# Optimization experiments

Measured on AMD Instinct MI355X. Metric: run time of the kernel, lower is better.

The kernel has to match this reference:

```python
import jax, jax.numpy as jnp
import numpy as np
import math

HIDDEN = 256
N_HEADS = 4
MAX_NB = 64  # max neighbors per sample (segment length cap)
B = 4096
N_TOTAL = 131072


def setup_inputs() -> dict:
    key = jax.random.key(0)
    ks = jax.random.split(key, 12)
    enc_hidden = jax.random.normal(ks[0], (B, HIDDEN), dtype=jnp.float32)
    social_ht = jax.random.normal(ks[1], (N_TOTAL, HIDDEN), dtype=jnp.float32)
    # contiguous ragged segments: start in [0, N_TOTAL-MAX_NB], len in [1, MAX_NB]
    starts = jnp.sort(jax.random.randint(ks[2], (B,), 0, N_TOTAL - MAX_NB, dtype=jnp.int32))
    lens = jax.random.randint(ks[3], (B,), 1, MAX_NB + 1, dtype=jnp.int32)
    ends = starts + lens
    s = 1.0 / math.sqrt(HIDDEN)
    def lin(k):
        kw, kb = jax.random.split(k)
        W = jax.random.uniform(kw, (HIDDEN, HIDDEN), jnp.float32, -s, s)
        b = jax.random.uniform(kb, (HIDDEN,), jnp.float32, -s, s)
        return W, b
    Wq, bq = lin(ks[4])
    Wk, bk = lin(ks[5])
    Wv, bv = lin(ks[6])
    Wf, bf = lin(ks[7])
    return {
        "enc_hidden": enc_hidden, "social_ht": social_ht,
        "Wq": Wq, "bq": bq, "Wk": Wk, "bk": bk, "Wv": Wv, "bv": bv,
        "Wf": Wf, "bf": bf,
        "neighbors_idx_start": starts, "neighbors_idx_end": ends,
    }


def reference(enc_hidden, social_ht, Wq, bq, Wk, bk, Wv, bv, Wf, bf,
              neighbors_idx_start, neighbors_idx_end):
    b, h = enc_hidden.shape
    dh = h // N_HEADS
    # query: Linear+ReLU then scale by sqrt(feat_dim) (as in source)
    q = jax.nn.relu(enc_hidden @ Wq.T + bq) / jnp.sqrt(jnp.float32(h))  # [B,H]
    # gather padded contiguous neighbor segments
    idx = neighbors_idx_start[:, None] + jnp.arange(MAX_NB, dtype=neighbors_idx_start.dtype)  # [B,M]
    valid = idx < neighbors_idx_end[:, None]  # [B,M]
    ht = social_ht[jnp.clip(idx, 0, social_ht.shape[0] - 1)]  # [B,M,H]
    k = jax.nn.relu(ht @ Wk.T + bk)  # [B,M,H]
    v = jax.nn.relu(ht @ Wv.T + bv)  # [B,M,H]
    qh = q.reshape(b, N_HEADS, dh)            # [B,h,d]
    kh = k.reshape(b, MAX_NB, N_HEADS, dh)    # [B,M,h,d]
    vh = v.reshape(b, MAX_NB, N_HEADS, dh)
    scores = jnp.einsum('bhd,bmhd->bhm', qh, kh)
    scores = jnp.where(valid[:, None, :], scores, jnp.float32(-1e30))
    attn = jax.nn.softmax(scores, axis=-1)    # [B,h,M]
    out = jnp.einsum('bhm,bmhd->bhd', attn, vh).reshape(b, h)
    return out @ Wf.T + bf
```

## Files before the change

kernel.cpp:

```cpp
#include <hip/hip_runtime.h>
#include <hip/hip_bf16.h>

typedef __attribute__((ext_vector_type(8))) short bf16x8;
typedef __attribute__((ext_vector_type(4))) float f32x4;
typedef __attribute__((ext_vector_type(4))) unsigned short us4;

__device__ __forceinline__ unsigned short f2bf(float f) {
    unsigned int u = __builtin_bit_cast(unsigned int, f);
    unsigned int r = (u + 0x7FFFu + ((u >> 16) & 1u)) >> 16;
    return (unsigned short)r;
}
__device__ __forceinline__ float bf2f(unsigned short h) {
    unsigned int u = ((unsigned int)h) << 16;
    return __builtin_bit_cast(float, u);
}

__device__ __forceinline__ void gload_lds16(const void* g, void* l) {
    __builtin_amdgcn_global_load_lds(
        (const __attribute__((address_space(1))) unsigned int*)g,
        (__attribute__((address_space(3))) unsigned int*)l, 16, 0, 0);
}

__global__ __launch_bounds__(512, 2) void kv_gemm_rb(
    const float* __restrict__ A,
    const float* __restrict__ Wk, const float* __restrict__ bk,
    const float* __restrict__ Wv, const float* __restrict__ bv,
    unsigned short* __restrict__ KV)
{
    __shared__ unsigned short Abuf[2][32 * 256];

    const int tid = threadIdx.x;
    const int wave = tid >> 6, lane = tid & 63;
    const size_t mb = (size_t)blockIdx.x * 512;

    bf16x8 bfrag[4][8];
    float biasv[4];
    #pragma unroll
    for (int ni = 0; ni < 4; ++ni) {
        int col = wave * 64 + ni * 16 + (lane & 15);
        const float* Wr = (col < 256) ? (Wk + (size_t)col * 256)
                                      : (Wv + (size_t)(col - 256) * 256);
        biasv[ni] = (col < 256) ? bk[col] : bv[col - 256];
        #pragma unroll
        for (int ks = 0; ks < 8; ++ks) {
            int k0 = ks * 32 + ((lane >> 4) << 3);
            float4 x = *(const float4*)(Wr + k0);
            float4 y = *(const float4*)(Wr + k0 + 4);
            bf16x8 f;
            f[0] = (short)f2bf(x.x); f[1] = (short)f2bf(x.y);
            f[2] = (short)f2bf(x.z); f[3] = (short)f2bf(x.w);
            f[4] = (short)f2bf(y.x); f[5] = (short)f2bf(y.y);
            f[6] = (short)f2bf(y.z); f[7] = (short)f2bf(y.w);
            bfrag[ni][ks] = f;
        }
    }

    {
        const int row = tid >> 4, seg = tid & 15;
        const float* src = A + (mb + row) * 256 + seg * 16;
        float4 a0 = *(const float4*)(src + 0);
        float4 a1 = *(const float4*)(src + 4);
        float4 a2 = *(const float4*)(src + 8);
        float4 a3 = *(const float4*)(src + 12);
        us4 h0, h1, h2, h3;
        h0.x=f2bf(a0.x); h0.y=f2bf(a0.y); h0.z=f2bf(a0.z); h0.w=f2bf(a0.w);
        h1.x=f2bf(a1.x); h1.y=f2bf(a1.y); h1.z=f2bf(a1.z); h1.w=f2bf(a1.w);
        h2.x=f2bf(a2.x); h2.y=f2bf(a2.y); h2.z=f2bf(a2.z); h2.w=f2bf(a2.w);
        h3.x=f2bf(a3.x); h3.y=f2bf(a3.y); h3.z=f2bf(a3.z); h3.w=f2bf(a3.w);
        char* dst = (char*)Abuf[0];
        int byte0 = row * 512 + seg * 32;
        int sw = (row & 7) << 4;
        *(us4*)(dst + ((byte0 +  0) ^ sw)) = h0;
        *(us4*)(dst + ((byte0 + 16) ^ sw)) = h1;
        *(us4*)(dst + ((byte0 + 0 + 16) ^ sw)) = h1;
        char* d2 = dst;
        *(us4*)(d2 + ((byte0 + 0) ^ sw)) = h0;
        *(us4*)(d2 + ((byte0 + 16) ^ sw)) = h1;
        *(us4*)(d2 + ((byte0 +  0) ^ sw)) = h0;
        *(us4*)(d2 + ((byte0 +  8) ^ sw)) = h1;
        *(us4*)(d2 + ((byte0 + 16) ^ sw)) = h2;
        *(us4*)(d2 + ((byte0 + 24) ^ sw)) = h3;
    }
    __syncthreads();

    for (int t = 0; t < 16; ++t) {
        const int cur = t & 1;
        const bool pf = (t + 1) < 16;
        float4 a0, a1, a2, a3;
        if (pf) {
            const int row = tid >> 4, seg = tid & 15;
            const float* src = A + (mb + (t + 1) * 32 + row) * 256 + seg * 16;
            a0 = *(const float4*)(src + 0);
            a1 = *(const float4*)(src + 4);
            a2 = *(const float4*)(src + 8);
            a3 = *(const float4*)(src + 12);
        }

        f32x4 acc[2][4] = {};
        const char* Ab = (const char*)Abuf[cur];
        #pragma unroll
        for (int ks = 0; ks < 8; ++ks) {
            bf16x8 af[2];
            #pragma unroll
            for (int mi = 0; mi < 2; ++mi) {
                int row = mi * 16 + (lane & 15);
                int byte = row * 512 + ks * 64 + ((lane >> 4) << 4);
                af[mi] = *(const bf16x8*)(Ab + (byte ^ ((row & 7) << 4)));
            }
            #pragma unroll
            for (int ni = 0; ni < 4; ++ni)
                #pragma unroll
                for (int mi = 0; mi < 2; ++mi)
                    acc[mi][ni] = __builtin_amdgcn_mfma_f32_16x16x32_bf16(
                        af[mi], bfrag[ni][ks], acc[mi][ni], 0, 0, 0);
        }

        #pragma unroll
        for (int ni = 0; ni < 4; ++ni) {
            int col = wave * 64 + ni * 16 + (lane & 15);
            #pragma unroll
            for (int mi = 0; mi < 2; ++mi) {
                size_t rbase = mb + (size_t)t * 32 + mi * 16 + ((lane >> 4) << 2);
                #pragma unroll
                for (int r = 0; r < 4; ++r) {
                    float v = fmaxf(acc[mi][ni][r] + biasv[ni], 0.f);
                    KV[(rbase + r) * 512 + col] = f2bf(v);
                }
            }
        }

        if (pf) {
            const int row = tid >> 4, seg = tid & 15;
            us4 h0, h1, h2, h3;
            h0.x=f2bf(a0.x); h0.y=f2bf(a0.y); h0.z=f2bf(a0.z); h0.w=f2bf(a0.w);
            h1.x=f2bf(a1.x); h1.y=f2bf(a1.y); h1.z=f2bf(a1.z); h1.w=f2bf(a1.w);
            h2.x=f2bf(a2.x); h2.y=f2bf(a2.y); h2.z=f2bf(a2.z); h2.w=f2bf(a2.w);
            h3.x=f2bf(a3.x); h3.y=f2bf(a3.y); h3.z=f2bf(a3.z); h3.w=f2bf(a3.w);
            char* dst = (char*)Abuf[cur ^ 1];
            int byte0 = row * 512 + seg * 32;
            int sw = (row & 7) << 4;
            *(us4*)(dst + ((byte0 +  0) ^ sw)) = h0;
            *(us4*)(dst + ((byte0 +  8) ^ sw)) = h1;
            *(us4*)(dst + ((byte0 + 16) ^ sw)) = h2;
            *(us4*)(dst + ((byte0 + 24) ^ sw)) = h3;
        }
        __syncthreads();
    }
}

template<int OUT_BF16, int RELU>
__global__ __launch_bounds__(256) void gemm_proj(
    const float* __restrict__ A, int M,
    const float* __restrict__ W0, const float* __restrict__ b0,
    const float* __restrict__ W1, const float* __restrict__ b1,
    void* __restrict__ outp, int ncol, float scale)
{
    __shared__ unsigned short As[128 * 64];
    __shared__ unsigned short Bs[64 * 64];
    char* AsB = (char*)As;
    char* BsB = (char*)Bs;

    const int tid = threadIdx.x;
    const int wave = tid >> 6, lane = tid & 63;
    const int m0 = blockIdx.x * 128;
    const int jbase = blockIdx.y * 64;

    f32x4 acc[2][4] = {};

    for (int kk = 0; kk < 256; kk += 64) {
        #pragma unroll
        for (int i = 0; i < 8; ++i) {
            int fidx = tid + i * 256;
            int row = fidx >> 4;
            int col4 = (fidx & 15) << 2;
            const float4 v = *(const float4*)(A + (size_t)(m0 + row) * 256 + kk + col4);
            us4 h; h.x = f2bf(v.x); h.y = f2bf(v.y); h.z = f2bf(v.z); h.w = f2bf(v.w);
            int byte = row * 128 + col4 * 2;
            *(us4*)(AsB + (byte ^ ((row & 7) << 4))) = h;
        }
        #pragma unroll
        for (int i = 0; i < 4; ++i) {
            int fidx = tid + i * 256;
            int row = fidx >> 4;
            int col4 = (fidx & 15) << 2;
            int j = jbase + row;
            const float* W = (j < 256) ? (W0 + (size_t)j * 256) : (W1 + (size_t)(j - 256) * 256);
            const float4 v = *(const float4*)(W + kk + col4);
            us4 h; h.x = f2bf(v.x); h.y = f2bf(v.y); h.z = f2bf(v.z); h.w = f2bf(v.w);
            int byte = row * 128 + col4 * 2;
            *(us4*)(BsB + (byte ^ ((row & 7) << 4))) = h;
        }
        __syncthreads();
        #pragma unroll
        for (int k2 = 0; k2 < 2; ++k2) {
            const int kbyte = k2 * 64 + ((lane >> 4) << 4);
            bf16x8 af[2];
            #pragma unroll
            for (int mi = 0; mi < 2; ++mi) {
                int row = wave * 32 + mi * 16 + (lane & 15);
                int byte = row * 128 + kbyte;
                af[mi] = *(const bf16x8*)(AsB + (byte ^ ((row & 7) << 4)));
            }
            #pragma unroll
            for (int ni = 0; ni < 4; ++ni) {
                int row = ni * 16 + (lane & 15);
                int byte = row * 128 + kbyte;
                bf16x8 bfr = *(const bf16x8*)(BsB + (byte ^ ((row & 7) << 4)));
                #pragma unroll
                for (int mi = 0; mi < 2; ++mi)
                    acc[mi][ni] = __builtin_amdgcn_mfma_f32_16x16x32_bf16(af[mi], bfr, acc[mi][ni], 0, 0, 0);
            }
        }
        __syncthreads();
    }

    #pragma unroll
    for (int ni = 0; ni < 4; ++ni) {
        int col = ni * 16 + (lane & 15);
        int j = jbase + col;
        float bias = (j < 256) ? b0[j] : b1[j - 256];
        #pragma unroll
        for (int mi = 0; mi < 2; ++mi) {
            int rbase = m0 + wave * 32 + mi * 16 + ((lane >> 4) << 2);
            #pragma unroll
            for (int r = 0; r < 4; ++r) {
                float v = acc[mi][ni][r] + bias;
                if (RELU) v = fmaxf(v, 0.f);
                v *= scale;
                size_t off = (size_t)(rbase + r) * ncol + j;
                if (OUT_BF16) ((unsigned short*)outp)[off] = f2bf(v);
                else ((float*)outp)[off] = v;
            }
        }
    }
}

__global__ __launch_bounds__(256) void attn_kernel(
    const float* __restrict__ Q, const unsigned short* __restrict__ KV,
    const int* __restrict__ starts, const int* __restrict__ ends,
    float* __restrict__ out)
{
    extern __shared__ char lds[];
    char* kv = lds;
    float* awl = (float*)(lds + 65536);
    float* qs  = (float*)(lds + 65536 + 1024);

    const int bid = blockIdx.x;
    const int b = ((bid & 7) << 9) + (bid >> 3);
    const int t = threadIdx.x;
    const int h = t >> 6, ln = t & 63;
    const int start = starts[b];
    const int len = ends[b] - start;

    #pragma unroll
    for (int i = 0; i < 16; ++i) {
        int r = h * 16 + i;
        const char* src = (const char*)KV + (size_t)(start + r) * 1024;
        int sb = (ln * 16) ^ ((r & 7) << 4);
        gload_lds16(src + sb, kv + r * 1024 + ln * 16);
    }
    qs[t] = Q[(size_t)b * 256 + t];
    __syncthreads();

    float2 qreg[32];
    #pragma unroll
    for (int j = 0; j < 32; ++j)
        qreg[j] = *(const float2*)(qs + h * 64 + 2 * j);

    float sx = 0.f, sy = 0.f;
    {
        const char* krow = kv + ln * 1024;
        const int sw = (ln & 7) << 4;
        #pragma unroll
        for (int j8 = 0; j8 < 8; ++j8) {
            bf16x8 kf = *(const bf16x8*)(krow + (((h * 128) + j8 * 16) ^ sw));
            #pragma unroll
            for (int p = 0; p < 4; ++p) {
                float2 q2 = qreg[j8 * 4 + p];
                sx = fmaf(q2.x, bf2f((unsigned short)kf[2 * p]), sx);
                sy = fmaf(q2.y, bf2f((unsigned short)kf[2 * p + 1]), sy);
            }
        }
    }
    float s = (ln < len) ? (sx + sy) : -3.0e38f;
    float mx = s;
    #pragma unroll
    for (int off = 32; off; off >>= 1) mx = fmaxf(mx, __shfl_xor(mx, off));
    float e = (ln < len) ? __expf(s - mx) : 0.f;
    float sum = e;
    #pragma unroll
    for (int off = 32; off; off >>= 1) sum += __shfl_xor(sum, off);
    awl[h * 64 + ln] = e / sum;
    __syncthreads();

    const int half = ln >> 5, dl = ln & 31;
    float a0 = 0.f, a1 = 0.f;
    {
        const char* vbase = kv + half * 32768;
        const int voff = 512 + h * 128 + dl * 4;
        #pragma unroll
        for (int mm = 0; mm < 32; ++mm) {
            unsigned int vv = *(const unsigned int*)(vbase + mm * 1024 + (voff ^ ((mm & 7) << 4)));
            float awm = awl[h * 64 + half * 32 + mm];
            float lo = __builtin_bit_cast(float, vv << 16);
            float hi = __builtin_bit_cast(float, vv & 0xFFFF0000u);
            a0 = fmaf(awm, lo, a0);
            a1 = fmaf(awm, hi, a1);
        }
    }
    a0 += __shfl_xor(a0, 32);
    a1 += __shfl_xor(a1, 32);
    if (ln < 32) {
        float2 o; o.x = a0; o.y = a1;
        *(float2*)(out + (size_t)b * 256 + h * 64 + 2 * dl) = o;
    }
}

extern "C" void kernel_launch(void* const* d_in, const int* in_sizes, int n_in,
                              void* d_out, int out_size, void* d_ws, size_t ws_size,
                              hipStream_t stream) {
    const float* enc    = (const float*)d_in[0];
    const float* social = (const float*)d_in[1];
    const float* Wq = (const float*)d_in[2];
    const float* bq = (const float*)d_in[3];
    const float* Wk = (const float*)d_in[4];
    const float* bk = (const float*)d_in[5];
    const float* Wv = (const float*)d_in[6];
    const float* bv = (const float*)d_in[7];
    const float* Wf = (const float*)d_in[8];
    const float* bf = (const float*)d_in[9];
    const int* st = (const int*)d_in[10];
    const int* en = (const int*)d_in[11];
    (void)in_sizes; (void)n_in; (void)out_size; (void)ws_size;

    char* ws = (char*)d_ws;
    unsigned short* KV = (unsigned short*)ws;
    float* Qb    = (float*)(ws + 134217728);
    float* attnb = (float*)(ws + 134217728 + 4194304);
    float* outf  = (float*)d_out;

    kv_gemm_rb<<<dim3(256), dim3(512), 0, stream>>>(social, Wk, bk, Wv, bv, KV);
    gemm_proj<0, 1><<<dim3(32, 4), dim3(256), 0, stream>>>(enc, 4096, Wq, bq, nullptr, nullptr, Qb, 256, 0.0625f);
    attn_kernel<<<dim3(4096), dim3(256), 67584, stream>>>(Qb, KV, st, en, attnb);
    gemm_proj<0, 0><<<dim3(32, 4), dim3(256), 0, stream>>>(attnb, 4096, Wf, bf, nullptr, nullptr, outf, 256, 1.0f);
}
```

Before: 318.6 us.

## Restructure KV layout per head, split GEMM columns, per-head attention blocks

The KV projection kernel now splits output columns across twice as many blocks and interleaves K and V per head. The MFMA operands are swapped so each lane writes four contiguous bf16 values, and the bias is loaded as a float4. Attention runs one 64-thread block per (batch, head), loading only that head's 256-byte KV slice and skipping rows beyond the segment length in both the gather and the V accumulation. The Q and output projections now stage the full K dimension in LDS once and store float4 results. Together these aim to cut redundant KV traffic and uncoalesced stores, at the cost of a data-dependent loop and smaller blocks.

```diff
diff --git a/kernel.cpp b/kernel.cpp
--- a/kernel.cpp
+++ b/kernel.cpp
@@ -21,26 +21,30 @@
         (__attribute__((address_space(3))) unsigned int*)l, 16, 0, 0);
 }
 
-__global__ __launch_bounds__(512, 2) void kv_gemm_rb(
+__global__ __launch_bounds__(512, 4) void kv_gemm_rb(
     const float* __restrict__ A,
     const float* __restrict__ Wk, const float* __restrict__ bk,
     const float* __restrict__ Wv, const float* __restrict__ bv,
-    unsigned short* __restrict__ KV)
+    unsigned short* __restrict__ KV2)
 {
     __shared__ unsigned short Abuf[2][32 * 256];
 
     const int tid = threadIdx.x;
     const int wave = tid >> 6, lane = tid & 63;
-    const size_t mb = (size_t)blockIdx.x * 512;
-
-    bf16x8 bfrag[4][8];
-    float biasv[4];
-    #pragma unroll
-    for (int ni = 0; ni < 4; ++ni) {
-        int col = wave * 64 + ni * 16 + (lane & 15);
-        const float* Wr = (col < 256) ? (Wk + (size_t)col * 256)
-                                      : (Wv + (size_t)(col - 256) * 256);
-        biasv[ni] = (col < 256) ? bk[col] : bv[col - 256];
+
+    const int g = (blockIdx.x & 7) * 128 + (blockIdx.x >> 3);
+    const int colhalf = g & 1;
+    const size_t mb = (size_t)(g >> 1) * 256;
+    const int colbase = colhalf * 256 + wave * 32;
+
+    bf16x8 bfrag[2][8];
+    float biasr[2][4];
+    int inner0[2];
+    #pragma unroll
+    for (int ni = 0; ni < 2; ++ni) {
+        int jcol = colbase + ni * 16 + (lane & 15);
+        const float* Wr = (jcol < 256) ? (Wk + (size_t)jcol * 256)
+                                       : (Wv + (size_t)(jcol - 256) * 256);
         #pragma unroll
         for (int ks = 0; ks < 8; ++ks) {
             int k0 = ks * 32 + ((lane >> 4) << 3);
@@ -53,11 +57,20 @@
             f[6] = (short)f2bf(y.z); f[7] = (short)f2bf(y.w);
             bfrag[ni][ks] = f;
         }
-    }
+        int j0 = colbase + ni * 16 + ((lane >> 4) << 2);
+        const float* bsrc = (j0 < 256) ? (bk + j0) : (bv + j0 - 256);
+        float4 bb = *(const float4*)bsrc;
+        biasr[ni][0] = bb.x; biasr[ni][1] = bb.y; biasr[ni][2] = bb.z; biasr[ni][3] = bb.w;
+        if (j0 < 256) inner0[ni] = (j0 >> 6) * 128 + (j0 & 63);
+        else { int t2 = j0 - 256; inner0[ni] = (t2 >> 6) * 128 + 64 + (t2 & 63); }
+    }
+
+    const int srow = tid >> 4, sseg = tid & 15;
+    const int sbyte0 = srow * 512 + sseg * 32;
+    const int ssw = (srow & 7) << 4;
 
     {
-        const int row = tid >> 4, seg = tid & 15;
-        const float* src = A + (mb + row) * 256 + seg * 16;
+        const float* src = A + (mb + srow) * 256 + sseg * 16;
         float4 a0 = *(const float4*)(src + 0);
         float4 a1 = *(const float4*)(src + 4);
         float4 a2 = *(const float4*)(src + 8);
@@ -68,36 +81,26 @@
         h2.x=f2bf(a2.x); h2.y=f2bf(a2.y); h2.z=f2bf(a2.z); h2.w=f2bf(a2.w);
         h3.x=f2bf(a3.x); h3.y=f2bf(a3.y); h3.z=f2bf(a3.z); h3.w=f2bf(a3.w);
         char* dst = (char*)Abuf[0];
-        int byte0 = row * 512 + seg * 32;
-        int sw = (row & 7) << 4;
-        *(us4*)(dst + ((byte0 +  0) ^ sw)) = h0;
-        *(us4*)(dst + ((byte0 + 16) ^ sw)) = h1;
-        *(us4*)(dst + ((byte0 + 0 + 16) ^ sw)) = h1;
-        char* d2 = dst;
-        *(us4*)(d2 + ((byte0 + 0) ^ sw)) = h0;
-        *(us4*)(d2 + ((byte0 + 16) ^ sw)) = h1;
-        *(us4*)(d2 + ((byte0 +  0) ^ sw)) = h0;
-        *(us4*)(d2 + ((byte0 +  8) ^ sw)) = h1;
-        *(us4*)(d2 + ((byte0 + 16) ^ sw)) = h2;
-        *(us4*)(d2 + ((byte0 + 24) ^ sw)) = h3;
+        *(us4*)(dst + ((sbyte0 +  0) ^ ssw)) = h0;
+        *(us4*)(dst + ((sbyte0 +  8) ^ ssw)) = h1;
+        *(us4*)(dst + ((sbyte0 + 16) ^ ssw)) = h2;
+        *(us4*)(dst + ((sbyte0 + 24) ^ ssw)) = h3;
     }
     __syncthreads();
 
-    for (int t = 0; t < 16; ++t) {
-        const int cur = t & 1;
-        const bool pf = (t + 1) < 16;
+    for (int t = 0; t < 8; ++t) {
+        const bool pf = (t + 1) < 8;
         float4 a0, a1, a2, a3;
         if (pf) {
-            const int row = tid >> 4, seg = tid & 15;
-            const float* src = A + (mb + (t + 1) * 32 + row) * 256 + seg * 16;
+            const float* src = A + (mb + (t + 1) * 32 + srow) * 256 + sseg * 16;
             a0 = *(const float4*)(src + 0);
             a1 = *(const float4*)(src + 4);
             a2 = *(const float4*)(src + 8);
             a3 = *(const float4*)(src + 12);
         }
 
-        f32x4 acc[2][4] = {};
-        const char* Ab = (const char*)Abuf[cur];
+        f32x4 acc[2][2] = {};
+        const char* Ab = (const char*)Abuf[t & 1];
         #pragma unroll
         for (int ks = 0; ks < 8; ++ks) {
             bf16x8 af[2];
@@ -108,172 +111,173 @@
                 af[mi] = *(const bf16x8*)(Ab + (byte ^ ((row & 7) << 4)));
             }
             #pragma unroll
-            for (int ni = 0; ni < 4; ++ni)
+            for (int ni = 0; ni < 2; ++ni)
                 #pragma unroll
                 for (int mi = 0; mi < 2; ++mi)
                     acc[mi][ni] = __builtin_amdgcn_mfma_f32_16x16x32_bf16(
-                        af[mi], bfrag[ni][ks], acc[mi][ni], 0, 0, 0);
-        }
-
-        #pragma unroll
-        for (int ni = 0; ni < 4; ++ni) {
-            int col = wave * 64 + ni * 16 + (lane & 15);
+                        bfrag[ni][ks], af[mi], acc[mi][ni], 0, 0, 0);
+        }
+
+        #pragma unroll
+        for (int ni = 0; ni < 2; ++ni) {
             #pragma unroll
             for (int mi = 0; mi < 2; ++mi) {
-                size_t rbase = mb + (size_t)t * 32 + mi * 16 + ((lane >> 4) << 2);
+                size_t m = mb + (size_t)t * 32 + mi * 16 + (lane & 15);
+                us4 h;
                 #pragma unroll
-                for (int r = 0; r < 4; ++r) {
-                    float v = fmaxf(acc[mi][ni][r] + biasv[ni], 0.f);
-                    KV[(rbase + r) * 512 + col] = f2bf(v);
-                }
+                for (int r = 0; r < 4; ++r)
+                    h[r] = f2bf(fmaxf(acc[mi][ni][r] + biasr[ni][r], 0.f));
+                *(us4*)(KV2 + m * 512 + inner0[ni]) = h;
             }
         }
 
         if (pf) {
-            const int row = tid >> 4, seg = tid & 15;
             us4 h0, h1, h2, h3;
             h0.x=f2bf(a0.x); h0.y=f2bf(a0.y); h0.z=f2bf(a0.z); h0.w=f2bf(a0.w);
             h1.x=f2bf(a1.x); h1.y=f2bf(a1.y); h1.z=f2bf(a1.z); h1.w=f2bf(a1.w);
             h2.x=f2bf(a2.x); h2.y=f2bf(a2.y); h2.z=f2bf(a2.z); h2.w=f2bf(a2.w);
             h3.x=f2bf(a3.x); h3.y=f2bf(a3.y); h3.z=f2bf(a3.z); h3.w=f2bf(a3.w);
-            char* dst = (char*)Abuf[cur ^ 1];
-            int byte0 = row * 512 + seg * 32;
-            int sw = (row & 7) << 4;
-            *(us4*)(dst + ((byte0 +  0) ^ sw)) = h0;
-            *(us4*)(dst + ((byte0 +  8) ^ sw)) = h1;
-            *(us4*)(dst + ((byte0 + 16) ^ sw)) = h2;
-            *(us4*)(dst + ((byte0 + 24) ^ sw)) = h3;
+            char* dst = (char*)Abuf[(t + 1) & 1];
+            *(us4*)(dst + ((sbyte0 +  0) ^ ssw)) = h0;
+            *(us4*)(dst + ((sbyte0 +  8) ^ ssw)) = h1;
+            *(us4*)(dst + ((sbyte0 + 16) ^ ssw)) = h2;
+            *(us4*)(dst + ((sbyte0 + 24) ^ ssw)) = h3;
         }
         __syncthreads();
     }
 }
 
-template<int OUT_BF16, int RELU>
+template<int RELU>
 __global__ __launch_bounds__(256) void gemm_proj(
-    const float* __restrict__ A, int M,
-    const float* __restrict__ W0, const float* __restrict__ b0,
-    const float* __restrict__ W1, const float* __restrict__ b1,
-    void* __restrict__ outp, int ncol, float scale)
+    const float* __restrict__ A, const float* __restrict__ W,
+    const float* __restrict__ bias, float* __restrict__ out, float scale)
 {
-    __shared__ unsigned short As[128 * 64];
-    __shared__ unsigned short Bs[64 * 64];
+    __shared__ unsigned short As[64 * 256];
+    __shared__ unsigned short Bs[64 * 256];
     char* AsB = (char*)As;
     char* BsB = (char*)Bs;
 
     const int tid = threadIdx.x;
     const int wave = tid >> 6, lane = tid & 63;
-    const int m0 = blockIdx.x * 128;
+    const int m0 = blockIdx.x * 64;
     const int jbase = blockIdx.y * 64;
 
-    f32x4 acc[2][4] = {};
-
-    for (int kk = 0; kk < 256; kk += 64) {
-        #pragma unroll
-        for (int i = 0; i < 8; ++i) {
-            int fidx = tid + i * 256;
-            int row = fidx >> 4;
-            int col4 = (fidx & 15) << 2;
-            const float4 v = *(const float4*)(A + (size_t)(m0 + row) * 256 + kk + col4);
-            us4 h; h.x = f2bf(v.x); h.y = f2bf(v.y); h.z = f2bf(v.z); h.w = f2bf(v.w);
-            int byte = row * 128 + col4 * 2;
-            *(us4*)(AsB + (byte ^ ((row & 7) << 4))) = h;
-        }
-        #pragma unroll
-        for (int i = 0; i < 4; ++i) {
-            int fidx = tid + i * 256;
-            int row = fidx >> 4;
-            int col4 = (fidx & 15) << 2;
-            int j = jbase + row;
-            const float* W = (j < 256) ? (W0 + (size_t)j * 256) : (W1 + (size_t)(j - 256) * 256);
-            const float4 v = *(const float4*)(W + kk + col4);
-            us4 h; h.x = f2bf(v.x); h.y = f2bf(v.y); h.z = f2bf(v.z); h.w = f2bf(v.w);
-            int byte = row * 128 + col4 * 2;
-            *(us4*)(BsB + (byte ^ ((row & 7) << 4))) = h;
-        }
-        __syncthreads();
-        #pragma unroll
-        for (int k2 = 0; k2 < 2; ++k2) {
-            const int kbyte = k2 * 64 + ((lane >> 4) << 4);
-            bf16x8 af[2];
-            #pragma unroll
-            for (int mi = 0; mi < 2; ++mi) {
-                int row = wave * 32 + mi * 16 + (lane & 15);
-                int byte = row * 128 + kbyte;
-                af[mi] = *(const bf16x8*)(AsB + (byte ^ ((row & 7) << 4)));
-            }
-            #pragma unroll
-            for (int ni = 0; ni < 4; ++ni) {
-                int row = ni * 16 + (lane & 15);
-                int byte = row * 128 + kbyte;
-                bf16x8 bfr = *(const bf16x8*)(BsB + (byte ^ ((row & 7) << 4)));
-                #pragma unroll
-                for (int mi = 0; mi < 2; ++mi)
-                    acc[mi][ni] = __builtin_amdgcn_mfma_f32_16x16x32_bf16(af[mi], bfr, acc[mi][ni], 0, 0, 0);
-            }
-        }
-        __syncthreads();
-    }
-
+    #pragma unroll
+    for (int i = 0; i < 4; ++i) {
+        int f = tid + i * 256;
+        int row = f >> 4, seg = f & 15;
+        int byte0 = row * 512 + seg * 32;
+        int sw = (row & 7) << 4;
+        {
+            const float* pa = A + (size_t)(m0 + row) * 256 + seg * 16;
+            float4 a0 = *(const float4*)(pa + 0);
+            float4 a1 = *(const float4*)(pa + 4);
+            float4 a2 = *(const float4*)(pa + 8);
+            float4 a3 = *(const float4*)(pa + 12);
+            us4 h0, h1, h2, h3;
+            h0.x=f2bf(a0.x); h0.y=f2bf(a0.y); h0.z=f2bf(a0.z); h0.w=f2bf(a0.w);
+            h1.x=f2bf(a1.x); h1.y=f2bf(a1.y); h1.z=f2bf(a1.z); h1.w=f2bf(a1.w);
+            h2.x=f2bf(a2.x); h2.y=f2bf(a2.y); h2.z=f2bf(a2.z); h2.w=f2bf(a2.w);
+            h3.x=f2bf(a3.x); h3.y=f2bf(a3.y); h3.z=f2bf(a3.z); h3.w=f2bf(a3.w);
+            *(us4*)(AsB + ((byte0 +  0) ^ sw)) = h0;
+            *(us4*)(AsB + ((byte0 +  8) ^ sw)) = h1;
+            *(us4*)(AsB + ((byte0 + 16) ^ sw)) = h2;
+            *(us4*)(AsB + ((byte0 + 24) ^ sw)) = h3;
+        }
+        {
+            const float* pw = W + (size_t)(jbase + row) * 256 + seg * 16;
+            float4 a0 = *(const float4*)(pw + 0);
+            float4 a1 = *(const float4*)(pw + 4);
+            float4 a2 = *(const float4*)(pw + 8);
+            float4 a3 = *(const float4*)(pw + 12);
+            us4 h0, h1, h2, h3;
+            h0.x=f2bf(a0.x); h0.y=f2bf(a0.y); h0.z=f2bf(a0.z); h0.w=f2bf(a0.w);
+            h1.x=f2bf(a1.x); h1.y=f2bf(a1.y); h1.z=f2bf(a1.z); h1.w=f2bf(a1.w);
+            h2.x=f2bf(a2.x); h2.y=f2bf(a2.y); h2.z=f2bf(a2.z); h2.w=f2bf(a2.w);
+            h3.x=f2bf(a3.x); h3.y=f2bf(a3.y); h3.z=f2bf(a3.z); h3.w=f2bf(a3.w);
+            *(us4*)(BsB + ((byte0 +  0) ^ sw)) = h0;
+            *(us4*)(BsB + ((byte0 +  8) ^ sw)) = h1;
+            *(us4*)(BsB + ((byte0 + 16) ^ sw)) = h2;
+            *(us4*)(BsB + ((byte0 + 24) ^ sw)) = h3;
+        }
+    }
+    __syncthreads();
+
+    f32x4 acc[4] = {};
+    #pragma unroll
+    for (int ks = 0; ks < 8; ++ks) {
+        int arow = wave * 16 + (lane & 15);
+        int abyte = arow * 512 + ks * 64 + ((lane >> 4) << 4);
+        bf16x8 af = *(const bf16x8*)(AsB + (abyte ^ ((arow & 7) << 4)));
+        #pragma unroll
+        for (int ni = 0; ni < 4; ++ni) {
+            int brow = ni * 16 + (lane & 15);
+            int bbyte = brow * 512 + ks * 64 + ((lane >> 4) << 4);
+            bf16x8 bfr = *(const bf16x8*)(BsB + (bbyte ^ ((brow & 7) << 4)));
+            acc[ni] = __builtin_amdgcn_mfma_f32_16x16x32_bf16(bfr, af, acc[ni], 0, 0, 0);
+        }
+    }
+
+    int m = m0 + wave * 16 + (lane & 15);
     #pragma unroll
     for (int ni = 0; ni < 4; ++ni) {
-        int col = ni * 16 + (lane & 15);
-        int j = jbase + col;
-        float bias = (j < 256) ? b0[j] : b1[j - 256];
-        #pragma unroll
-        for (int mi = 0; mi < 2; ++mi) {
-            int rbase = m0 + wave * 32 + mi * 16 + ((lane >> 4) << 2);
-            #pragma unroll
-            for (int r = 0; r < 4; ++r) {
-                float v = acc[mi][ni][r] + bias;
-                if (RELU) v = fmaxf(v, 0.f);
-                v *= scale;
-                size_t off = (size_t)(rbase + r) * ncol + j;
-                if (OUT_BF16) ((unsigned short*)outp)[off] = f2bf(v);
-                else ((float*)outp)[off] = v;
-            }
-        }
-    }
-}
-
-__global__ __launch_bounds__(256) void attn_kernel(
-    const float* __restrict__ Q, const unsigned short* __restrict__ KV,
+        int j0 = jbase + ni * 16 + ((lane >> 4) << 2);
+        float4 bb = *(const float4*)(bias + j0);
+        float4 o;
+        o.x = acc[ni][0] + bb.x; o.y = acc[ni][1] + bb.y;
+        o.z = acc[ni][2] + bb.z; o.w = acc[ni][3] + bb.w;
+        if (RELU) {
+            o.x = fmaxf(o.x, 0.f); o.y = fmaxf(o.y, 0.f);
+            o.z = fmaxf(o.z, 0.f); o.w = fmaxf(o.w, 0.f);
+        }
+        o.x *= scale; o.y *= scale; o.z *= scale; o.w *= scale;
+        *(float4*)(out + (size_t)m * 256 + j0) = o;
+    }
+}
+
+__global__ __launch_bounds__(64) void attn_kernel(
+    const float* __restrict__ Q, const unsigned short* __restrict__ KV2,
     const int* __restrict__ starts, const int* __restrict__ ends,
     float* __restrict__ out)
 {
-    extern __shared__ char lds[];
-    char* kv = lds;
-    float* awl = (float*)(lds + 65536);
-    float* qs  = (float*)(lds + 65536 + 1024);
+    __shared__ unsigned short kvs[64 * 128];
+    __shared__ float qs[64];
+    __shared__ float aw[64];
 
     const int bid = blockIdx.x;
-    const int b = ((bid & 7) << 9) + (bid >> 3);
-    const int t = threadIdx.x;
-    const int h = t >> 6, ln = t & 63;
+    const int idx = ((bid & 7) << 11) | (bid >> 3);
+    const int b = idx >> 2, h = idx & 3;
+    const int ln = threadIdx.x;
     const int start = starts[b];
     const int len = ends[b] - start;
 
-    #pragma unroll
-    for (int i = 0; i < 16; ++i) {
-        int r = h * 16 + i;
-        const char* src = (const char*)KV + (size_t)(start + r) * 1024;
-        int sb = (ln * 16) ^ ((r & 7) << 4);
-        gload_lds16(src + sb, kv + r * 1024 + ln * 16);
-    }
-    qs[t] = Q[(size_t)b * 256 + t];
+    {
+        const int r4 = ln >> 4, c = ln & 15;
+        #pragma unroll
+        for (int i = 0; i < 16; ++i) {
+            if (i * 4 < len) {
+                int rr = i * 4 + r4;
+                const char* src = (const char*)(KV2 + (size_t)(start + rr) * 512 + h * 128)
+                                  + ((c * 16) ^ ((rr & 7) << 4));
+                gload_lds16(src, (char*)kvs + i * 1024 + ln * 16);
+            }
+        }
+    }
+    qs[ln] = Q[(size_t)b * 256 + h * 64 + ln];
     __syncthreads();
 
     float2 qreg[32];
     #pragma unroll
     for (int j = 0; j < 32; ++j)
-        qreg[j] = *(const float2*)(qs + h * 64 + 2 * j);
+        qreg[j] = *(const float2*)(qs + 2 * j);
 
     float sx = 0.f, sy = 0.f;
     {
-        const char* krow = kv + ln * 1024;
+        const char* krow = (const char*)kvs + ln * 256;
         const int sw = (ln & 7) << 4;
         #pragma unroll
         for (int j8 = 0; j8 < 8; ++j8) {
-            bf16x8 kf = *(const bf16x8*)(krow + (((h * 128) + j8 * 16) ^ sw));
+            bf16x8 kf = *(const bf16x8*)(krow + ((j8 * 16) ^ sw));
             #pragma unroll
             for (int p = 0; p < 4; ++p) {
                 float2 q2 = qreg[j8 * 4 + p];
@@ -290,23 +294,19 @@
     float sum = e;
     #pragma unroll
     for (int off = 32; off; off >>= 1) sum += __shfl_xor(sum, off);
-    awl[h * 64 + ln] = e / sum;
+    aw[ln] = e / sum;
     __syncthreads();
 
     const int half = ln >> 5, dl = ln & 31;
+    int nm = len - half * 32; nm = nm < 0 ? 0 : (nm > 32 ? 32 : nm);
     float a0 = 0.f, a1 = 0.f;
-    {
-        const char* vbase = kv + half * 32768;
-        const int voff = 512 + h * 128 + dl * 4;
-        #pragma unroll
-        for (int mm = 0; mm < 32; ++mm) {
-            unsigned int vv = *(const unsigned int*)(vbase + mm * 1024 + (voff ^ ((mm & 7) << 4)));
-            float awm = awl[h * 64 + half * 32 + mm];
-            float lo = __builtin_bit_cast(float, vv << 16);
-            float hi = __builtin_bit_cast(float, vv & 0xFFFF0000u);
-            a0 = fmaf(awm, lo, a0);
-            a1 = fmaf(awm, hi, a1);
-        }
+    const char* vb = (const char*)kvs + half * 32 * 256;
+    const int voff = 128 + dl * 4;
+    for (int mm = 0; mm < nm; ++mm) {
+        unsigned int vv = *(const unsigned int*)(vb + mm * 256 + (voff ^ ((mm & 7) << 4)));
+        float awm = aw[half * 32 + mm];
+        a0 = fmaf(awm, __builtin_bit_cast(float, vv << 16), a0);
+        a1 = fmaf(awm, __builtin_bit_cast(float, vv & 0xFFFF0000u), a1);
     }
     a0 += __shfl_xor(a0, 32);
     a1 += __shfl_xor(a1, 32);
@@ -334,13 +334,13 @@
     (void)in_sizes; (void)n_in; (void)out_size; (void)ws_size;
 
     char* ws = (char*)d_ws;
-    unsigned short* KV = (unsigned short*)ws;
+    unsigned short* KV2 = (unsigned short*)ws;
     float* Qb    = (float*)(ws + 134217728);
     float* attnb = (float*)(ws + 134217728 + 4194304);
     float* outf  = (float*)d_out;
 
-    kv_gemm_rb<<<dim3(256), dim3(512), 0, stream>>>(social, Wk, bk, Wv, bv, KV);
-    gemm_proj<0, 1><<<dim3(32, 4), dim3(256), 0, stream>>>(enc, 4096, Wq, bq, nullptr, nullptr, Qb, 256, 0.0625f);
-    attn_kernel<<<dim3(4096), dim3(256), 67584, stream>>>(Qb, KV, st, en, attnb);
-    gemm_proj<0, 0><<<dim3(32, 4), dim3(256), 0, stream>>>(attnb, 4096, Wf, bf, nullptr, nullptr, outf, 256, 1.0f);
-}
+    kv_gemm_rb<<<dim3(1024), dim3(512), 0, stream>>>(social, Wk, bk, Wv, bv, KV2);
+    gemm_proj<1><<<dim3(64, 4), dim3(256), 0, stream>>>(enc, Wq, bq, Qb, 0.0625f);
+    attn_kernel<<<dim3(16384), dim3(64), 0, stream>>>(Qb, KV2, st, en, attnb);
+    gemm_proj<0><<<dim3(64, 4), dim3(256), 0, stream>>>(attnb, Wf, bf, outf, 1.0f);
+}
```

Measured after the change: 355.7 us. +11.7%, slower.
